# Kernel optimization log

Measured on AMD Instinct MI355X. Metric: run time of the kernel, lower is better.

## Reference

```python
import jax, jax.numpy as jnp
import numpy as np

B, S, D_IN, D_OUT = 8, 4096, 1024, 1024
R_F, R_M, R_S = 8, 32, 64
R_TOT = R_F + R_M + R_S  # 104
HID = 64
ALPHA = 1.0


def setup_inputs() -> dict:
    key = jax.random.key(0)
    ks = jax.random.split(key, 10)
    inp = {
        "x": jax.random.normal(ks[0], (B, S, D_IN), dtype=jnp.float32),
        # fresh memory state after reset_memory(): zeros of shape [batch, r_*]
        "mem_fast": jnp.zeros((B, R_F), dtype=jnp.float32),
        "mem_medium": jnp.zeros((B, R_M), dtype=jnp.float32),
        "mem_slow": jnp.zeros((B, R_S), dtype=jnp.float32),
        # frozen base nn.Linear
        "base_w": jax.random.normal(ks[1], (D_OUT, D_IN), dtype=jnp.float32) / np.sqrt(D_IN),
        "base_b": jax.random.normal(ks[2], (D_OUT,), dtype=jnp.float32) * 0.01,
        # LoRA projections: proj_down kaiming-ish, proj_up zero-init per _init_weights
        "pd_w": jax.random.normal(ks[3], (R_TOT, D_IN), dtype=jnp.float32) / np.sqrt(D_IN),
        "pu_w": jax.random.normal(ks[4], (D_OUT, R_TOT), dtype=jnp.float32) * 0.01,
        # gate_net: Linear(D_IN, HID) -> GELU -> Linear(HID, 3) -> Softmax
        "g1_w": jax.random.normal(ks[5], (HID, D_IN), dtype=jnp.float32) / np.sqrt(D_IN),
        "g1_b": jnp.zeros((HID,), dtype=jnp.float32),
        "g2_w": jax.random.normal(ks[6], (3, HID), dtype=jnp.float32) / np.sqrt(HID),
        "g2_b": jnp.zeros((3,), dtype=jnp.float32),
    }
    return inp


def reference(x, mem_fast, mem_medium, mem_slow, base_w, base_b,
              pd_w, pu_w, g1_w, g1_b, g2_w, g2_b):
    # base linear: [B,S,D_out]
    base_out = jnp.einsum("bsd,od->bso", x, base_w) + base_b
    # down projection: [B,S,R_TOT]
    proj = jnp.einsum("bsd,rd->bsr", x, pd_w)
    # per-timescale multiplicative modulation by recurrent memory state
    # (split -> (1+mem)*proj -> concat) == concat memories once
    mem = jnp.concatenate([mem_fast, mem_medium, mem_slow], axis=-1)  # [B,R_TOT]
    modulated = proj * (1.0 + mem[:, None, :])
    # gate_net: Linear -> GELU(exact) -> Linear -> softmax over 3 timescales
    h = jax.nn.gelu(jnp.einsum("bsd,hd->bsh", x, g1_w) + g1_b, approximate=False)
    gates = jax.nn.softmax(jnp.einsum("bsh,gh->bsg", h, g2_w) + g2_b, axis=-1)
    gate_scale = jnp.mean(gates, axis=-1, keepdims=True)  # [B,S,1]
    # up projection and residual combine
    lora_out = jnp.einsum("bsr,or->bso", modulated, pu_w)
    output = base_out + ALPHA * lora_out * gate_scale
    return output
```

## Files before the change

kernel.cpp:

```cpp
#include <hip/hip_runtime.h>
#include <stdint.h>


typedef unsigned short ushort_t;
typedef unsigned short us8 __attribute__((ext_vector_type(8)));
typedef short short8 __attribute__((ext_vector_type(8)));
typedef float f32x4 __attribute__((ext_vector_type(4)));

__device__ __forceinline__ ushort_t f2b(float f) {
  union { float f; uint32_t i; } v; v.f = f;
  uint32_t lsb = (v.i >> 16) & 1u;
  v.i += 0x7fffu + lsb;
  return (ushort_t)(v.i >> 16);
}

__device__ __forceinline__ void async16(const void* g, void* l) {
  __builtin_amdgcn_global_load_lds(
      (const __attribute__((address_space(1))) void*)g,
      (__attribute__((address_space(3))) void*)l, 16, 0, 0);
}

__global__ __launch_bounds__(256) void convert_x(const float* __restrict__ x,
                                                 ushort_t* __restrict__ xb) {
  const int flat = blockIdx.x;
  const int b = flat & 7;
  const int c0 = flat >> 3;
  const size_t base = (size_t)b * 4194304 + (size_t)c0 * 16384;
#pragma unroll 2
  for (int u = 0; u < 8; ++u) {
    const size_t i = base + u * 2048 + threadIdx.x * 8;
    f32x4 a0 = *(const f32x4*)(x + i);
    f32x4 a1 = *(const f32x4*)(x + i + 4);
    us8 o;
#pragma unroll
    for (int j = 0; j < 4; j++) { o[j] = f2b(a0[j]); o[4 + j] = f2b(a1[j]); }
    *(us8*)(xb + i) = o;
  }
}

__global__ __launch_bounds__(128) void prep(const float* __restrict__ base_w,
                                            const float* __restrict__ pu_w,
                                            const float* __restrict__ pd_w,
                                            const float* __restrict__ mf,
                                            const float* __restrict__ mm,
                                            const float* __restrict__ ms,
                                            ushort_t* __restrict__ W0,
                                            ushort_t* __restrict__ Weff,
                                            int* __restrict__ flags) {
  const int o = blockIdx.x, y = blockIdx.y, t = threadIdx.x;
  __shared__ float spu[104];
  __shared__ int sflag;
  ushort_t* dst;

  if (y == 0) {
    if (t < 104) spu[t] = pu_w[o * 104 + t] * (1.0f / 3.0f);
    dst = W0 + o * 1024;
    __syncthreads();
  } else {
    const int b = y - 1;
    if (t == 0) sflag = 0;
    __syncthreads();
    float mv = 0.0f;
    if (t < 104) {
      mv = (t < 8) ? mf[b * 8 + t]
         : (t < 40) ? mm[b * 32 + (t - 8)]
                    : ms[b * 64 + (t - 40)];
      if (mv != 0.0f) sflag = 1;
      spu[t] = pu_w[o * 104 + t] * (1.0f + mv) * (1.0f / 3.0f);
    }
    __syncthreads();
    if (o == 0 && t == 0) flags[b] = sflag;
    if (!sflag) return;
    dst = Weff + ((size_t)b << 20) + o * 1024;
  }

  const int d0 = t * 8;
  float acc[8];
  f32x4 b0 = *(const f32x4*)(base_w + o * 1024 + d0);
  f32x4 b1 = *(const f32x4*)(base_w + o * 1024 + d0 + 4);
#pragma unroll
  for (int j = 0; j < 4; j++) { acc[j] = b0[j]; acc[4 + j] = b1[j]; }
  for (int r = 0; r < 104; r++) {
    f32x4 p0 = *(const f32x4*)(pd_w + r * 1024 + d0);
    f32x4 p1 = *(const f32x4*)(pd_w + r * 1024 + d0 + 4);
    float s = spu[r];
#pragma unroll
    for (int j = 0; j < 4; j++) { acc[j] += s * p0[j]; acc[4 + j] += s * p1[j]; }
  }
  us8 ov;
#pragma unroll
  for (int j = 0; j < 8; j++) ov[j] = f2b(acc[j]);
  *(us8*)(dst + d0) = ov;
}

__global__ __launch_bounds__(512, 2) void gemm256(
    const ushort_t* __restrict__ xb, const float* __restrict__ base_b,
    const ushort_t* __restrict__ W0, const ushort_t* __restrict__ Weff,
    const int* __restrict__ flags, float* __restrict__ out) {
  const int flat = blockIdx.x;
  const int b  = flat & 7;
  const int i  = flat >> 3;
  const int bm = i >> 2;
  const int bn = i & 3;

  const ushort_t* W = flags[b] ? (Weff + ((size_t)b << 20)) : W0;

  __shared__ __align__(16) char lds[4 * 32768];

  const int t = threadIdx.x;
  const int w = t >> 6, l = t & 63;
  const int wr = w >> 2, wc = w & 3;
  const int row16 = l & 15, quad = l >> 4;

  const int srow = w * 16 + (l >> 2);
  const int scol = (((l & 3) ^ ((l >> 3) & 3))) * 8;
  const ushort_t* gA = xb + (((size_t)b * 4096 + bm * 256 + srow) << 10) + scol;
  const ushort_t* gB = W + (((size_t)(bn * 256 + srow)) << 10) + scol;

  const int qsw = (quad ^ ((row16 >> 1) & 3)) * 16;
  const int aoff = (wr * 128 + row16) * 64 + qsw;
  const int boff = 16384 + (wc * 64 + row16) * 64 + qsw;

#define STAGE_A(kt)                                                       \
  {                                                                       \
    const ushort_t* g_ = gA + (kt) * 32;                                  \
    char* d_ = lds + ((kt) & 3) * 32768 + w * 1024;                       \
    async16(g_, d_);                                                      \
    async16(g_ + (128 << 10), d_ + 8192);                                 \
  }
#define STAGE_B(kt)                                                       \
  {                                                                       \
    const ushort_t* g_ = gB + (kt) * 32;                                  \
    char* d_ = lds + ((kt) & 3) * 32768 + 16384 + w * 1024;               \
    async16(g_, d_);                                                      \
    async16(g_ + (128 << 10), d_ + 8192);                                 \
  }

  f32x4 acc[8][4] = {};
  short8 af[2][4], bf[2][4], af2[4];

  STAGE_A(0) STAGE_B(0) STAGE_A(1) STAGE_B(1)
  asm volatile("s_waitcnt vmcnt(4)" ::: "memory");
  __builtin_amdgcn_s_barrier();
#pragma unroll
  for (int mi = 0; mi < 4; ++mi)
    af[0][mi] = *(const short8*)(lds + aoff + mi * 1024);
#pragma unroll
  for (int ni = 0; ni < 4; ++ni)
    bf[0][ni] = *(const short8*)(lds + boff + ni * 1024);

#pragma unroll 4
  for (int kt = 0; kt < 32; ++kt) {
    const int p = kt & 1;
    const char* cur = lds + (kt & 3) * 32768;
    const char* nxt = lds + ((kt + 1) & 3) * 32768;

    if (kt < 30) STAGE_A(kt + 2)
#pragma unroll
    for (int j = 0; j < 4; ++j)
      af2[j] = *(const short8*)(cur + aoff + (4 + j) * 1024);
    __builtin_amdgcn_s_setprio(1);
#pragma unroll
    for (int mi = 0; mi < 4; ++mi)
#pragma unroll
      for (int ni = 0; ni < 4; ++ni)
        acc[mi][ni] = __builtin_amdgcn_mfma_f32_16x16x32_bf16(af[p][mi], bf[p][ni],
                                                              acc[mi][ni], 0, 0, 0);
    __builtin_amdgcn_s_setprio(0);

    if (kt < 30) {
      asm volatile("s_waitcnt vmcnt(2)" ::: "memory");
    } else if (kt == 30) {
      asm volatile("s_waitcnt vmcnt(0)" ::: "memory");
    }
    __builtin_amdgcn_s_barrier();

    if (kt < 30) STAGE_B(kt + 2)
    if (kt < 31) {
#pragma unroll
      for (int mi = 0; mi < 4; ++mi)
        af[p ^ 1][mi] = *(const short8*)(nxt + aoff + mi * 1024);
#pragma unroll
      for (int ni = 0; ni < 4; ++ni)
        bf[p ^ 1][ni] = *(const short8*)(nxt + boff + ni * 1024);
    }
    __builtin_amdgcn_s_setprio(1);
#pragma unroll
    for (int mi = 0; mi < 4; ++mi)
#pragma unroll
      for (int ni = 0; ni < 4; ++ni)
        acc[4 + mi][ni] = __builtin_amdgcn_mfma_f32_16x16x32_bf16(af2[mi], bf[p][ni],
                                                                  acc[4 + mi][ni], 0, 0, 0);
    __builtin_amdgcn_s_setprio(0);
  }

#pragma unroll
  for (int ni = 0; ni < 4; ++ni) {
    const int col = bn * 256 + wc * 64 + ni * 16 + row16;
    const float bb = base_b[col];
#pragma unroll
    for (int mi = 0; mi < 8; ++mi) {
      const int row = bm * 256 + wr * 128 + mi * 16 + quad * 4;
      float* po = out + (((size_t)b * 4096 + row) << 10) + col;
#pragma unroll
      for (int i2 = 0; i2 < 4; ++i2)
        po[(size_t)i2 << 10] = acc[mi][ni][i2] + bb;
    }
  }
#undef STAGE_A
#undef STAGE_B
}

extern "C" void kernel_launch(void* const* d_in, const int* in_sizes, int n_in,
                              void* d_out, int out_size, void* d_ws, size_t ws_size,
                              hipStream_t stream) {
  const float* x  = (const float*)d_in[0];
  const float* mf = (const float*)d_in[1];
  const float* mm = (const float*)d_in[2];
  const float* ms = (const float*)d_in[3];
  const float* base_w = (const float*)d_in[4];
  const float* base_b = (const float*)d_in[5];
  const float* pd_w = (const float*)d_in[6];
  const float* pu_w = (const float*)d_in[7];

  char* ws = (char*)d_ws;
  int* flags     = (int*)ws;
  ushort_t* W0   = (ushort_t*)(ws + 4096);
  ushort_t* xb   = (ushort_t*)(ws + 4096 + (2u << 20));
  ushort_t* Weff = (ushort_t*)(ws + 4096 + (2u << 20) + (64u << 20));

  prep<<<dim3(1024, 9), 128, 0, stream>>>(base_w, pu_w, pd_w, mf, mm, ms,
                                          W0, Weff, flags);
  convert_x<<<2048, 256, 0, stream>>>(x, xb);
  gemm256<<<512, 512, 0, stream>>>(xb, base_b, W0, Weff, flags, (float*)d_out);
}
```

Measured before the change: 408.0 us.

## Restructure GEMM main loop into barrier-separated phases and flatten x conversion

The GEMM main loop drops the register double-buffering of A/B fragments across iterations. Each k-step now loads its fragments from the current LDS stage, issues async copies for stage k+2, and runs two MFMA halves separated by sched_barrier plus s_barrier, with a vmcnt(4) wait at the end. This aims to give the scheduler a simpler pattern and to reduce register pressure, at the cost of extra barriers and less overlap of LDS reads with MFMA. Separately, convert_x is changed to one 8-element chunk per thread over 16384 blocks instead of a loop of 8 per thread.

```diff
diff --git a/kernel.cpp b/kernel.cpp
--- a/kernel.cpp
+++ b/kernel.cpp
@@ -24,18 +24,14 @@
                                                  ushort_t* __restrict__ xb) {
   const int flat = blockIdx.x;
   const int b = flat & 7;
-  const int c0 = flat >> 3;
-  const size_t base = (size_t)b * 4194304 + (size_t)c0 * 16384;
-#pragma unroll 2
-  for (int u = 0; u < 8; ++u) {
-    const size_t i = base + u * 2048 + threadIdx.x * 8;
-    f32x4 a0 = *(const f32x4*)(x + i);
-    f32x4 a1 = *(const f32x4*)(x + i + 4);
-    us8 o;
-#pragma unroll
-    for (int j = 0; j < 4; j++) { o[j] = f2b(a0[j]); o[4 + j] = f2b(a1[j]); }
-    *(us8*)(xb + i) = o;
-  }
+  const int c = flat >> 3;
+  const size_t i = (((size_t)b * 2048 + c) * 256 + threadIdx.x) * 8;
+  f32x4 a0 = *(const f32x4*)(x + i);
+  f32x4 a1 = *(const f32x4*)(x + i + 4);
+  us8 o;
+#pragma unroll
+  for (int j = 0; j < 4; j++) { o[j] = f2b(a0[j]); o[4 + j] = f2b(a1[j]); }
+  *(us8*)(xb + i) = o;
 }
 
 __global__ __launch_bounds__(128) void prep(const float* __restrict__ base_w,
@@ -137,61 +133,55 @@
   }
 
   f32x4 acc[8][4] = {};
-  short8 af[2][4], bf[2][4], af2[4];
 
   STAGE_A(0) STAGE_B(0) STAGE_A(1) STAGE_B(1)
   asm volatile("s_waitcnt vmcnt(4)" ::: "memory");
   __builtin_amdgcn_s_barrier();
-#pragma unroll
-  for (int mi = 0; mi < 4; ++mi)
-    af[0][mi] = *(const short8*)(lds + aoff + mi * 1024);
-#pragma unroll
-  for (int ni = 0; ni < 4; ++ni)
-    bf[0][ni] = *(const short8*)(lds + boff + ni * 1024);
-
-#pragma unroll 4
+
   for (int kt = 0; kt < 32; ++kt) {
-    const int p = kt & 1;
     const char* cur = lds + (kt & 3) * 32768;
-    const char* nxt = lds + ((kt + 1) & 3) * 32768;
-
+
+    short8 af[4], bf[4];
+#pragma unroll
+    for (int mi = 0; mi < 4; ++mi)
+      af[mi] = *(const short8*)(cur + aoff + mi * 1024);
+#pragma unroll
+    for (int ni = 0; ni < 4; ++ni)
+      bf[ni] = *(const short8*)(cur + boff + ni * 1024);
     if (kt < 30) STAGE_A(kt + 2)
-#pragma unroll
-    for (int j = 0; j < 4; ++j)
-      af2[j] = *(const short8*)(cur + aoff + (4 + j) * 1024);
+    __builtin_amdgcn_sched_barrier(0);
+    __builtin_amdgcn_s_barrier();
     __builtin_amdgcn_s_setprio(1);
 #pragma unroll
     for (int mi = 0; mi < 4; ++mi)
 #pragma unroll
       for (int ni = 0; ni < 4; ++ni)
-        acc[mi][ni] = __builtin_amdgcn_mfma_f32_16x16x32_bf16(af[p][mi], bf[p][ni],
+        acc[mi][ni] = __builtin_amdgcn_mfma_f32_16x16x32_bf16(af[mi], bf[ni],
                                                               acc[mi][ni], 0, 0, 0);
     __builtin_amdgcn_s_setprio(0);
 
+    short8 af2[4];
+#pragma unroll
+    for (int mi = 0; mi < 4; ++mi)
+      af2[mi] = *(const short8*)(cur + aoff + (4 + mi) * 1024);
+    if (kt < 30) STAGE_B(kt + 2)
+    __builtin_amdgcn_sched_barrier(0);
+    __builtin_amdgcn_s_barrier();
+    __builtin_amdgcn_s_setprio(1);
+#pragma unroll
+    for (int mi = 0; mi < 4; ++mi)
+#pragma unroll
+      for (int ni = 0; ni < 4; ++ni)
+        acc[4 + mi][ni] = __builtin_amdgcn_mfma_f32_16x16x32_bf16(af2[mi], bf[ni],
+                                                                  acc[4 + mi][ni], 0, 0, 0);
+    __builtin_amdgcn_s_setprio(0);
+
     if (kt < 30) {
-      asm volatile("s_waitcnt vmcnt(2)" ::: "memory");
+      asm volatile("s_waitcnt vmcnt(4)" ::: "memory");
     } else if (kt == 30) {
       asm volatile("s_waitcnt vmcnt(0)" ::: "memory");
     }
     __builtin_amdgcn_s_barrier();
-
-    if (kt < 30) STAGE_B(kt + 2)
-    if (kt < 31) {
-#pragma unroll
-      for (int mi = 0; mi < 4; ++mi)
-        af[p ^ 1][mi] = *(const short8*)(nxt + aoff + mi * 1024);
-#pragma unroll
-      for (int ni = 0; ni < 4; ++ni)
-        bf[p ^ 1][ni] = *(const short8*)(nxt + boff + ni * 1024);
-    }
-    __builtin_amdgcn_s_setprio(1);
-#pragma unroll
-    for (int mi = 0; mi < 4; ++mi)
-#pragma unroll
-      for (int ni = 0; ni < 4; ++ni)
-        acc[4 + mi][ni] = __builtin_amdgcn_mfma_f32_16x16x32_bf16(af2[mi], bf[p][ni],
-                                                                  acc[4 + mi][ni], 0, 0, 0);
-    __builtin_amdgcn_s_setprio(0);
   }
 
 #pragma unroll
@@ -231,6 +221,6 @@
 
   prep<<<dim3(1024, 9), 128, 0, stream>>>(base_w, pu_w, pd_w, mf, mm, ms,
                                           W0, Weff, flags);
-  convert_x<<<2048, 256, 0, stream>>>(x, xb);
+  convert_x<<<16384, 256, 0, stream>>>(x, xb);
   gemm256<<<512, 512, 0, stream>>>(xb, base_b, W0, Weff, flags, (float*)d_out);
 }
```

Measured after the change: 344.2 us. 1.19x faster.
